# Optimization experiments

Measured on AMD Instinct MI355X. Metric: run time of the kernel, lower is better.

## Reference

```python
import jax, jax.numpy as jnp
import numpy as np


def trident(w, thresholds, noise_sd, noise):
    # thresholded + noised ternarization to {-1, 0, +1}
    wn = w + noise_sd * noise
    return jnp.where(wn < thresholds[0], -1.0, jnp.where(wn > thresholds[1], 1.0, 0.0)).astype(w.dtype)


def setup_inputs() -> dict:
    key = jax.random.key(0)
    k1, k2, k3, k4 = jax.random.split(key, 4)
    B, in_features, num_experts, expert_size = 8192, 4096, 64, 128
    in_chunks = in_features // expert_size  # 32
    x = jax.random.normal(k1, (B, in_features), dtype=jnp.float32)
    # glorot-like scaling for params
    routing_matrix = jax.random.normal(k2, (in_chunks, num_experts), dtype=jnp.float32) * np.sqrt(2.0 / (in_chunks + num_experts))
    We = jax.random.normal(k3, (num_experts, expert_size, expert_size), dtype=jnp.float32) * np.sqrt(1.0 / expert_size)
    noise = jax.random.normal(k4, (in_chunks, num_experts), dtype=jnp.float32)
    return {"x": x, "routing_matrix": routing_matrix, "We": We, "noise": noise}


def reference(x, routing_matrix, We, noise):
    thresholds = (-0.5, 0.5)
    noise_sd = 0.1
    expert_size = We.shape[-1]
    B = x.shape[0]
    xc = x.reshape(B, -1, expert_size)                     # (B, in_chunks, d)
    ternary = trident(routing_matrix, thresholds, noise_sd, noise)  # (in_chunks, E)
    x_routed = jnp.einsum('ik,bij->bkj', ternary, xc)      # (B, E, d)
    x_experts = jnp.einsum('eij,bej->bei', We, x_routed)   # (B, E, d)
    return x_experts.reshape(B, -1)
```

## Files before the change

### kernel.cpp

```cpp
#include <hip/hip_runtime.h>

#define IC   32
#define NE   64
#define D    128
#define IF   4096
#define OF   8192
#define TB   128

typedef float vf4 __attribute__((ext_vector_type(4)));

#define NNZ_OFF    0
#define NACT_OFF   64
#define ACT_OFF    65
#define INACT_OFF  129
#define CHUNK_OFF  193
#define SIGN_OFF   (193 + NE * IC)

__global__ void prep_kernel(const float* __restrict__ routing,
                            const float* __restrict__ noise,
                            int* __restrict__ ws) {
    __shared__ float s_sign[IC][NE];
    const int t = threadIdx.x;

    #pragma unroll
    for (int i = 0; i < IC; ++i) {
        float w  = routing[i * NE + t];
        float nz = noise[i * NE + t];
        float wn = __fadd_rn(w, __fmul_rn(0.1f, nz));
        s_sign[i][t] = (wn < -0.5f) ? -1.0f : ((wn > 0.5f) ? 1.0f : 0.0f);
    }
    __syncthreads();

    int cnt = 0;
    #pragma unroll
    for (int i = 0; i < IC; ++i) {
        float sgn = s_sign[i][t];
        if (sgn != 0.0f) {
            ws[CHUNK_OFF + t * IC + cnt] = i;
            ((float*)ws)[SIGN_OFF + t * IC + cnt] = sgn;
            ++cnt;
        }
    }
    ws[NNZ_OFF + t] = cnt;

    unsigned long long mask = __ballot(cnt > 0);
    unsigned long long below = mask & ((t == 0) ? 0ull : (~0ull >> (64 - t)));
    int act_before = (int)__popcll(below);
    if (cnt > 0) ws[ACT_OFF + act_before] = t;
    else         ws[INACT_OFF + (t - act_before)] = t;
    if (t == 0)  ws[NACT_OFF] = (int)__popcll(mask);
}

__global__ __launch_bounds__(256, 1)
void main_kernel(const float* __restrict__ x,
                 const float* __restrict__ We,
                 const int* __restrict__ ws,
                 float* __restrict__ out) {
    __shared__ float sWe[D * D];
    __shared__ float sXr[TB * D];
    __shared__ int   s_chunk[IC];
    __shared__ float s_csign[IC];

    const int t  = threadIdx.x;
    const int bt = blockIdx.x;
    const int s  = blockIdx.y;
    const int nact = ws[NACT_OFF];

    const int c4 = t & 31;
    const int r0 = t >> 5;
    float4* out4 = (float4*)out;
    const size_t orow4 = OF / 4;

    if (s >= nact) {
        const int e = ws[INACT_OFF + (s - nact)];
        vf4* outv = (vf4*)out;
        const vf4 z = (vf4){0.f, 0.f, 0.f, 0.f};
        #pragma unroll
        for (int p = 0; p < TB / 8; ++p) {
            size_t row = (size_t)(bt * TB + p * 8 + r0);
            __builtin_nontemporal_store(z, &outv[row * orow4 + e * (D / 4) + c4]);
        }
        return;
    }

    const int e   = ws[ACT_OFF + s];
    const int nnz = ws[NNZ_OFF + e];
    if (t < nnz) {
        s_chunk[t] = ws[CHUNK_OFF + e * IC + t];
        s_csign[t] = ((const float*)ws)[SIGN_OFF + e * IC + t];
    }
    __syncthreads();

    const float4* We4 = (const float4*)(We + (size_t)e * D * D);
    #pragma unroll
    for (int p = 0; p < D / 8; ++p) {
        int r = p * 8 + r0;
        float4 w4 = We4[r * (D / 4) + c4];
        float wv[4] = {w4.x, w4.y, w4.z, w4.w};
        #pragma unroll
        for (int k = 0; k < 4; ++k) {
            int j = c4 * 4 + k;
            int blk = (r >> 3) ^ ((j >> 2) & 15);
            sWe[j * D + blk * 8 + (r & 7)] = wv[k];
        }
    }

    const float4* x4p = (const float4*)x;
    const size_t xrow4 = IF / 4;
    #pragma unroll
    for (int p = 0; p < TB / 8; ++p) {
        int b = p * 8 + r0;
        size_t row = (size_t)(bt * TB + b);
        float4 acc = make_float4(0.f, 0.f, 0.f, 0.f);
        for (int m = 0; m < nnz; ++m) {
            int   i  = s_chunk[m];
            float sg = s_csign[m];
            float4 v = x4p[row * xrow4 + i * (D / 4) + c4];
            acc.x += sg * v.x; acc.y += sg * v.y;
            acc.z += sg * v.z; acc.w += sg * v.w;
        }
        float av[4] = {acc.x, acc.y, acc.z, acc.w};
        #pragma unroll
        for (int k = 0; k < 4; ++k) {
            int j = c4 * 4 + k;
            int blk = (b >> 3) ^ ((j >> 2) & 15);
            sXr[j * TB + blk * 8 + (b & 7)] = av[k];
        }
    }
    __syncthreads();

    const int rg = t & 15;
    const int bg = t >> 4;
    float acc[8][8];
    #pragma unroll
    for (int a = 0; a < 8; ++a)
        #pragma unroll
        for (int c = 0; c < 8; ++c) acc[a][c] = 0.f;

    #pragma unroll 2
    for (int j = 0; j < D; ++j) {
        const int sw = (j >> 2) & 15;
        const float4* wr = (const float4*)&sWe[j * D  + ((rg ^ sw) << 3)];
        const float4* xr = (const float4*)&sXr[j * TB + ((bg ^ sw) << 3)];
        float4 w0 = wr[0], w1 = wr[1];
        float4 x0 = xr[0], x1 = xr[1];
        float wv[8] = {w0.x, w0.y, w0.z, w0.w, w1.x, w1.y, w1.z, w1.w};
        float xv[8] = {x0.x, x0.y, x0.z, x0.w, x1.x, x1.y, x1.z, x1.w};
        #pragma unroll
        for (int a = 0; a < 8; ++a)
            #pragma unroll
            for (int c = 0; c < 8; ++c)
                acc[a][c] += wv[a] * xv[c];
    }

    #pragma unroll
    for (int c = 0; c < 8; ++c) {
        size_t row  = (size_t)(bt * TB + bg * 8 + c);
        size_t base = row * orow4 + e * (D / 4) + rg * 2;
        out4[base]     = make_float4(acc[0][c], acc[1][c], acc[2][c], acc[3][c]);
        out4[base + 1] = make_float4(acc[4][c], acc[5][c], acc[6][c], acc[7][c]);
    }
}

extern "C" void kernel_launch(void* const* d_in, const int* in_sizes, int n_in,
                              void* d_out, int out_size, void* d_ws, size_t ws_size,
                              hipStream_t stream) {
    const float* x       = (const float*)d_in[0];
    const float* routing = (const float*)d_in[1];
    const float* We      = (const float*)d_in[2];
    const float* noise   = (const float*)d_in[3];
    float* out = (float*)d_out;
    int*   ws  = (int*)d_ws;

    const int B = in_sizes[0] / IF;

    prep_kernel<<<1, 64, 0, stream>>>(routing, noise, ws);
    dim3 grid(B / TB, NE);
    main_kernel<<<grid, 256, 0, stream>>>(x, We, ws, out);
}
```

Measured before the change: 431.1 us.

## Split reduction dim into two halves to halve LDS and allow two blocks per CU

The K dimension (128) of the per-expert GEMM is split into two 64-wide halves, so the shared-memory tiles for We and routed x shrink from 128 KB to 64 KB. The launch bounds change from one to two blocks per CU so two workgroups can co-reside and hide global-load latency. In exchange there is an extra barrier, x rows are loaded in two half-row passes, and tighter register limits could cause spills of the 64-float accumulator.

Measured after the change: 400.1 us. -7.2%, faster.

```diff
diff --git a/kernel.cpp b/kernel.cpp
--- a/kernel.cpp
+++ b/kernel.cpp
@@ -6,6 +6,7 @@
 #define IF   4096
 #define OF   8192
 #define TB   128
+#define KH   64
 
 typedef float vf4 __attribute__((ext_vector_type(4)));
 
@@ -51,13 +52,13 @@
     if (t == 0)  ws[NACT_OFF] = (int)__popcll(mask);
 }
 
-__global__ __launch_bounds__(256, 1)
+__global__ __launch_bounds__(256, 2)
 void main_kernel(const float* __restrict__ x,
                  const float* __restrict__ We,
                  const int* __restrict__ ws,
                  float* __restrict__ out) {
-    __shared__ float sWe[D * D];
-    __shared__ float sXr[TB * D];
+    __shared__ float sWe[KH * D];
+    __shared__ float sXr[KH * TB];
     __shared__ int   s_chunk[IC];
     __shared__ float s_csign[IC];
 
@@ -66,13 +67,13 @@
     const int s  = blockIdx.y;
     const int nact = ws[NACT_OFF];
 
-    const int c4 = t & 31;
-    const int r0 = t >> 5;
     float4* out4 = (float4*)out;
     const size_t orow4 = OF / 4;
 
     if (s >= nact) {
         const int e = ws[INACT_OFF + (s - nact)];
+        const int c4 = t & 31;
+        const int r0 = t >> 5;
         vf4* outv = (vf4*)out;
         const vf4 z = (vf4){0.f, 0.f, 0.f, 0.f};
         #pragma unroll
@@ -91,66 +92,74 @@
     }
     __syncthreads();
 
+    const int c4h = t & 15;
+    const int r0h = t >> 4;
+    const int rg  = t & 15;
+    const int bg  = t >> 4;
+
     const float4* We4 = (const float4*)(We + (size_t)e * D * D);
-    #pragma unroll
-    for (int p = 0; p < D / 8; ++p) {
-        int r = p * 8 + r0;
-        float4 w4 = We4[r * (D / 4) + c4];
-        float wv[4] = {w4.x, w4.y, w4.z, w4.w};
-        #pragma unroll
-        for (int k = 0; k < 4; ++k) {
-            int j = c4 * 4 + k;
-            int blk = (r >> 3) ^ ((j >> 2) & 15);
-            sWe[j * D + blk * 8 + (r & 7)] = wv[k];
-        }
-    }
+    const float4* x4p = (const float4*)x;
 
-    const float4* x4p = (const float4*)x;
-    const size_t xrow4 = IF / 4;
-    #pragma unroll
-    for (int p = 0; p < TB / 8; ++p) {
-        int b = p * 8 + r0;
-        size_t row = (size_t)(bt * TB + b);
-        float4 acc = make_float4(0.f, 0.f, 0.f, 0.f);
-        for (int m = 0; m < nnz; ++m) {
-            int   i  = s_chunk[m];
-            float sg = s_csign[m];
-            float4 v = x4p[row * xrow4 + i * (D / 4) + c4];
-            acc.x += sg * v.x; acc.y += sg * v.y;
-            acc.z += sg * v.z; acc.w += sg * v.w;
-        }
-        float av[4] = {acc.x, acc.y, acc.z, acc.w};
-        #pragma unroll
-        for (int k = 0; k < 4; ++k) {
-            int j = c4 * 4 + k;
-            int blk = (b >> 3) ^ ((j >> 2) & 15);
-            sXr[j * TB + blk * 8 + (b & 7)] = av[k];
-        }
-    }
-    __syncthreads();
-
-    const int rg = t & 15;
-    const int bg = t >> 4;
     float acc[8][8];
     #pragma unroll
     for (int a = 0; a < 8; ++a)
         #pragma unroll
         for (int c = 0; c < 8; ++c) acc[a][c] = 0.f;
 
-    #pragma unroll 2
-    for (int j = 0; j < D; ++j) {
-        const int sw = (j >> 2) & 15;
-        const float4* wr = (const float4*)&sWe[j * D  + ((rg ^ sw) << 3)];
-        const float4* xr = (const float4*)&sXr[j * TB + ((bg ^ sw) << 3)];
-        float4 w0 = wr[0], w1 = wr[1];
-        float4 x0 = xr[0], x1 = xr[1];
-        float wv[8] = {w0.x, w0.y, w0.z, w0.w, w1.x, w1.y, w1.z, w1.w};
-        float xv[8] = {x0.x, x0.y, x0.z, x0.w, x1.x, x1.y, x1.z, x1.w};
+    #pragma unroll
+    for (int h = 0; h < 2; ++h) {
+        if (h) __syncthreads();
+
         #pragma unroll
-        for (int a = 0; a < 8; ++a)
+        for (int p = 0; p < 8; ++p) {
+            int r = p * 16 + r0h;
+            float4 w4 = We4[r * (D / 4) + h * (KH / 4) + c4h];
+            float wv[4] = {w4.x, w4.y, w4.z, w4.w};
             #pragma unroll
-            for (int c = 0; c < 8; ++c)
-                acc[a][c] += wv[a] * xv[c];
+            for (int k = 0; k < 4; ++k) {
+                int jl  = c4h * 4 + k;
+                int blk = (r >> 3) ^ ((jl >> 2) & 15);
+                sWe[jl * D + blk * 8 + (r & 7)] = wv[k];
+            }
+        }
+
+        #pragma unroll
+        for (int p = 0; p < 8; ++p) {
+            int b = p * 16 + r0h;
+            size_t row = (size_t)(bt * TB + b);
+            float4 acc4 = make_float4(0.f, 0.f, 0.f, 0.f);
+            for (int m = 0; m < nnz; ++m) {
+                int   i  = s_chunk[m];
+                float sg = s_csign[m];
+                float4 v = x4p[row * (IF / 4) + i * (D / 4) + h * (KH / 4) + c4h];
+                acc4.x += sg * v.x; acc4.y += sg * v.y;
+                acc4.z += sg * v.z; acc4.w += sg * v.w;
+            }
+            float av[4] = {acc4.x, acc4.y, acc4.z, acc4.w};
+            #pragma unroll
+            for (int k = 0; k < 4; ++k) {
+                int jl  = c4h * 4 + k;
+                int blk = (b >> 3) ^ ((jl >> 2) & 15);
+                sXr[jl * TB + blk * 8 + (b & 7)] = av[k];
+            }
+        }
+        __syncthreads();
+
+        #pragma unroll 2
+        for (int jl = 0; jl < KH; ++jl) {
+            const int sw = (jl >> 2) & 15;
+            const float4* wr = (const float4*)&sWe[jl * D  + ((rg ^ sw) << 3)];
+            const float4* xr = (const float4*)&sXr[jl * TB + ((bg ^ sw) << 3)];
+            float4 w0 = wr[0], w1 = wr[1];
+            float4 x0 = xr[0], x1 = xr[1];
+            float wv[8] = {w0.x, w0.y, w0.z, w0.w, w1.x, w1.y, w1.z, w1.w};
+            float xv[8] = {x0.x, x0.y, x0.z, x0.w, x1.x, x1.y, x1.z, x1.w};
+            #pragma unroll
+            for (int a = 0; a < 8; ++a)
+                #pragma unroll
+                for (int c = 0; c < 8; ++c)
+                    acc[a][c] += wv[a] * xv[c];
+        }
     }
 
     #pragma unroll
```
